# Kernel optimization log

Measured on AMD Instinct MI355X. Metric: run time of the kernel, lower is better.

Reference implementation:

```python
import jax, jax.numpy as jnp
import numpy as np

H = 4          # no_heads
C_HIDDEN = 32  # per-head hidden dim


def setup_inputs() -> dict:
    key = jax.random.key(0)
    ks = jax.random.split(key, 11)
    B, S, C = 1, 256, 128
    sc = 1.0 / np.sqrt(C).astype(np.float32)
    return {
        "q_x": jax.random.normal(ks[0], (B, S, S, C), jnp.float32),
        "kv_x": jax.random.normal(ks[1], (B, S, S, C), jnp.float32),
        "bias1": jax.random.normal(ks[2], (B, 1, H, S, S), jnp.float32),
        "bias2": jax.random.normal(ks[3], (B, S, 1, 1, S), jnp.float32),
        "wq": jax.random.normal(ks[4], (C, C), jnp.float32) * sc,
        "wk": jax.random.normal(ks[5], (C, C), jnp.float32) * sc,
        "wv": jax.random.normal(ks[6], (C, C), jnp.float32) * sc,
        "wg": jax.random.normal(ks[7], (C, C), jnp.float32) * sc,
        "bg": jax.random.normal(ks[8], (C,), jnp.float32) * 0.02,
        "wo": jax.random.normal(ks[9], (C, C), jnp.float32) * sc,
        "bo": jax.random.normal(ks[10], (C,), jnp.float32) * 0.02,
    }


def reference(q_x, kv_x, bias1, bias2, wq, wk, wv, wg, bg, wo, bo):
    # Linear projections (torch Linear semantics: x @ W^T), no bias on q/k/v.
    def split_heads(x):  # ... Q (H C) -> ... H Q C
        *lead, Q, _ = x.shape
        return jnp.moveaxis(x.reshape(*lead, Q, H, C_HIDDEN), -2, -3)

    q = split_heads(jnp.einsum('...qi,oi->...qo', q_x, wq)) / np.sqrt(C_HIDDEN)
    k = split_heads(jnp.einsum('...ki,oi->...ko', kv_x, wk))
    v = split_heads(jnp.einsum('...ki,oi->...ko', kv_x, wv))

    # scores: [B, S, H, Q, K]
    a = jnp.einsum('bshqd,bshkd->bshqk', q, k)
    a = a + bias1 + bias2
    a = jax.nn.softmax(a, axis=-1)
    o = jnp.einsum('bshqk,bshkd->bshqd', a, v)
    o = jnp.moveaxis(o, -3, -2)  # ... H Q C -> ... Q H C

    # sigmoid gating
    g = jax.nn.sigmoid(jnp.einsum('...qi,oi->...qo', q_x, wg) + bg)
    *lead, Q, _ = g.shape
    g = g.reshape(*lead, Q, H, C_HIDDEN)
    o = o * g

    o = o.reshape(*lead, Q, H * C_HIDDEN)
    return jnp.einsum('...qi,oi->...qo', o, wo) + bo
```

## Files before the change

kernel.cpp:

```cpp
#include <hip/hip_runtime.h>
#include <math.h>

typedef _Float16 f16;
typedef _Float16 h4 __attribute__((ext_vector_type(4)));
typedef _Float16 h8 __attribute__((ext_vector_type(8)));
typedef float f32x4 __attribute__((ext_vector_type(4)));

#define QSCALE 0.17677669529663689f

__global__ __launch_bounds__(256) void proj_mfma(
    const float* __restrict__ q_x, const float* __restrict__ kv_x,
    const float* __restrict__ wq, const float* __restrict__ wk,
    const float* __restrict__ wv, const float* __restrict__ wg,
    const float* __restrict__ bg,
    f16* __restrict__ qb, f16* __restrict__ kb,
    f16* __restrict__ vbT, f16* __restrict__ gb)
{
    __shared__ char lds[65536];
    char* xl = lds;
    char* wl = lds + 32768;
    const int t = threadIdx.x;
    const int lane = t & 63, wave = t >> 6;
    const int wr = wave >> 1, wc = wave & 1;
    const int lo = lane & 15, hi = lane >> 4;
    const int phase = blockIdx.y;
    const int row0 = blockIdx.x * 128;
    const float* xsrc = phase ? kv_x : q_x;

    #pragma unroll
    for (int j = 0; j < 16; ++j) {
        int f = t + 256 * j;
        int row = f >> 5, c4 = f & 31;
        float4 v = *(const float4*)(xsrc + (size_t)(row0 + row) * 128 + c4 * 4);
        h4 hv = {(f16)v.x, (f16)v.y, (f16)v.z, (f16)v.w};
        *(h4*)(xl + row * 256 + (((c4 >> 1) ^ (row & 7)) << 4) + ((c4 & 1) << 3)) = hv;
    }

    for (int sub = 0; sub < 2; ++sub) {
        const int pid = phase * 2 + sub;
        const float* w = (pid == 0) ? wq : (pid == 1) ? wg : (pid == 2) ? wk : wv;
        __syncthreads();
        #pragma unroll
        for (int j = 0; j < 16; ++j) {
            int f = t + 256 * j;
            int row = f >> 5, c4 = f & 31;
            float4 v = *(const float4*)(w + (size_t)row * 128 + c4 * 4);
            h4 hv = {(f16)v.x, (f16)v.y, (f16)v.z, (f16)v.w};
            *(h4*)(wl + row * 256 + (((c4 >> 1) ^ (row & 7)) << 4) + ((c4 & 1) << 3)) = hv;
        }
        __syncthreads();

        f32x4 acc[4][4];
        #pragma unroll
        for (int m = 0; m < 4; ++m)
            #pragma unroll
            for (int n = 0; n < 4; ++n) acc[m][n] = (f32x4){0.f, 0.f, 0.f, 0.f};

        #pragma unroll
        for (int kk = 0; kk < 4; ++kk) {
            const int swz = ((hi + 4 * kk) ^ (lo & 7)) << 4;
            h8 af[4], bf[4];
            #pragma unroll
            for (int m = 0; m < 4; ++m)
                af[m] = *(const h8*)(xl + (lo + 16 * m + 64 * wr) * 256 + swz);
            #pragma unroll
            for (int n = 0; n < 4; ++n)
                bf[n] = *(const h8*)(wl + (lo + 16 * n + 64 * wc) * 256 + swz);
            #pragma unroll
            for (int m = 0; m < 4; ++m)
                #pragma unroll
                for (int n = 0; n < 4; ++n)
                    acc[m][n] = __builtin_amdgcn_mfma_f32_16x16x32_f16(af[m], bf[n], acc[m][n], 0, 0, 0);
        }

        #pragma unroll
        for (int n = 0; n < 4; ++n) {
            const int col = 64 * wc + 16 * n + lo;
            const float bgv = (pid == 1) ? bg[col] : 0.f;
            #pragma unroll
            for (int m = 0; m < 4; ++m) {
                if (pid == 3) {
                    int rg = row0 + 64 * wr + 16 * m + 4 * hi;
                    int sidx = rg >> 8, key = rg & 255;
                    int hh = col >> 5, dh = col & 31;
                    h4 hv = {(f16)acc[m][n][0], (f16)acc[m][n][1],
                             (f16)acc[m][n][2], (f16)acc[m][n][3]};
                    *(h4*)(vbT + (((size_t)sidx * 4 + hh) * 32 + dh) * 256 + key) = hv;
                } else {
                    f16* dst = (pid == 0) ? qb : (pid == 1) ? gb : kb;
                    #pragma unroll
                    for (int r = 0; r < 4; ++r) {
                        int rg = row0 + 64 * wr + 16 * m + 4 * hi + r;
                        float v = acc[m][n][r];
                        if (pid == 0) v *= QSCALE;
                        else if (pid == 1) v = 1.f / (1.f + __expf(-(v + bgv)));
                        dst[(size_t)rg * 128 + col] = (f16)v;
                    }
                }
            }
        }
    }
}

__global__ __launch_bounds__(256) void attn_mfma(
    const f16* __restrict__ qb, const f16* __restrict__ kb,
    const f16* __restrict__ vbT, const f16* __restrict__ gb,
    const float* __restrict__ bias1, const float* __restrict__ bias2,
    f16* __restrict__ ob)
{
    __shared__ char plds[16384];
    const int h = blockIdx.x, s = blockIdx.y;
    const int t = threadIdx.x, wave = t >> 6, lane = t & 63;
    const int lo = lane & 15, hi = lane >> 4;
    char* pw = plds + wave * 4096;
    const size_t rowbase = (size_t)s * 256;
    const int q0 = wave * 64;

    h8 qf[4];
    #pragma unroll
    for (int m = 0; m < 4; ++m)
        qf[m] = *(const h8*)(qb + (rowbase + q0 + 16 * m + lo) * 128 + h * 32 + 8 * hi);

    f32x4 Oa[4][2];
    float mr[4][4], lr[4][4];
    #pragma unroll
    for (int m = 0; m < 4; ++m) {
        #pragma unroll
        for (int n = 0; n < 2; ++n) Oa[m][n] = (f32x4){0.f, 0.f, 0.f, 0.f};
        #pragma unroll
        for (int r = 0; r < 4; ++r) { mr[m][r] = -1e30f; lr[m][r] = 0.f; }
    }

    const float* b1 = bias1 + (size_t)h * 65536;
    const float* b2 = bias2 + (size_t)s * 256;
    const f16* vbase = vbT + ((size_t)s * 4 + h) * 32 * 256;

    for (int k0 = 0; k0 < 256; k0 += 32) {
        h8 kf[2];
        #pragma unroll
        for (int nt = 0; nt < 2; ++nt)
            kf[nt] = *(const h8*)(kb + (rowbase + k0 + 16 * nt + lo) * 128 + h * 32 + 8 * hi);
        float b2v[2];
        #pragma unroll
        for (int nt = 0; nt < 2; ++nt) b2v[nt] = b2[k0 + 16 * nt + lo];

        f32x4 acc[4][2];
        #pragma unroll
        for (int m = 0; m < 4; ++m)
            #pragma unroll
            for (int nt = 0; nt < 2; ++nt)
                #pragma unroll
                for (int r = 0; r < 4; ++r)
                    acc[m][nt][r] = b1[(q0 + 16 * m + 4 * hi + r) * 256 + k0 + 16 * nt + lo] + b2v[nt];

        #pragma unroll
        for (int m = 0; m < 4; ++m)
            #pragma unroll
            for (int nt = 0; nt < 2; ++nt)
                acc[m][nt] = __builtin_amdgcn_mfma_f32_16x16x32_f16(qf[m], kf[nt], acc[m][nt], 0, 0, 0);

        float corr[4][4];
        #pragma unroll
        for (int m = 0; m < 4; ++m) {
            #pragma unroll
            for (int r = 0; r < 4; ++r) {
                float mx = fmaxf(acc[m][0][r], acc[m][1][r]);
                #pragma unroll
                for (int wdt = 1; wdt < 16; wdt <<= 1)
                    mx = fmaxf(mx, __shfl_xor(mx, wdt, 16));
                float mn = fmaxf(mr[m][r], mx);
                corr[m][r] = __expf(mr[m][r] - mn);
                mr[m][r] = mn;
                float p0 = __expf(acc[m][0][r] - mn);
                float p1 = __expf(acc[m][1][r] - mn);
                acc[m][0][r] = p0;
                acc[m][1][r] = p1;
                float sm = p0 + p1;
                #pragma unroll
                for (int wdt = 1; wdt < 16; wdt <<= 1)
                    sm += __shfl_xor(sm, wdt, 16);
                lr[m][r] = lr[m][r] * corr[m][r] + sm;
            }
        }

        #pragma unroll
        for (int m = 0; m < 4; ++m)
            #pragma unroll
            for (int nt = 0; nt < 2; ++nt)
                #pragma unroll
                for (int r = 0; r < 4; ++r) {
                    int q = 16 * m + 4 * hi + r;
                    int swz = (nt * 2 + (lo >> 3)) ^ r ^ hi;
                    *(f16*)(pw + q * 64 + swz * 16 + (lo & 7) * 2) = (f16)acc[m][nt][r];
                }

        #pragma unroll
        for (int m = 0; m < 4; ++m)
            #pragma unroll
            for (int n2 = 0; n2 < 2; ++n2)
                #pragma unroll
                for (int r = 0; r < 4; ++r)
                    Oa[m][n2][r] *= corr[m][r];

        h8 vf[2];
        #pragma unroll
        for (int n2 = 0; n2 < 2; ++n2)
            vf[n2] = *(const h8*)(vbase + (n2 * 16 + lo) * 256 + k0 + 8 * hi);

        #pragma unroll
        for (int m = 0; m < 4; ++m) {
            int swz = hi ^ (lo & 3) ^ ((lo >> 2) & 3);
            h8 pa = *(const h8*)(pw + (16 * m + lo) * 64 + (swz << 4));
            #pragma unroll
            for (int n2 = 0; n2 < 2; ++n2)
                Oa[m][n2] = __builtin_amdgcn_mfma_f32_16x16x32_f16(pa, vf[n2], Oa[m][n2], 0, 0, 0);
        }
    }

    #pragma unroll
    for (int m = 0; m < 4; ++m) {
        #pragma unroll
        for (int r = 0; r < 4; ++r) {
            float inv = 1.f / lr[m][r];
            int qg = q0 + 16 * m + 4 * hi + r;
            #pragma unroll
            for (int n2 = 0; n2 < 2; ++n2) {
                size_t idx = (rowbase + qg) * 128 + h * 32 + n2 * 16 + lo;
                float g = (float)gb[idx];
                ob[idx] = (f16)(Oa[m][n2][r] * inv * g);
            }
        }
    }
}

__global__ __launch_bounds__(256) void out_mfma(
    const f16* __restrict__ ob, const float* __restrict__ wo,
    const float* __restrict__ bo, float* __restrict__ out)
{
    __shared__ char lds[65536];
    char* xl = lds;
    char* wl = lds + 32768;
    const int t = threadIdx.x;
    const int lane = t & 63, wave = t >> 6;
    const int wr = wave >> 1, wc = wave & 1;
    const int lo = lane & 15, hi = lane >> 4;
    const int row0 = blockIdx.x * 128;

    #pragma unroll
    for (int j = 0; j < 8; ++j) {
        int f = t + 256 * j;
        int row = f >> 4, c8 = f & 15;
        h8 v = *(const h8*)(ob + (size_t)(row0 + row) * 128 + c8 * 8);
        *(h8*)(xl + row * 256 + ((c8 ^ (row & 7)) << 4)) = v;
    }
    #pragma unroll
    for (int j = 0; j < 16; ++j) {
        int f = t + 256 * j;
        int row = f >> 5, c4 = f & 31;
        float4 v = *(const float4*)(wo + (size_t)row * 128 + c4 * 4);
        h4 hv = {(f16)v.x, (f16)v.y, (f16)v.z, (f16)v.w};
        *(h4*)(wl + row * 256 + (((c4 >> 1) ^ (row & 7)) << 4) + ((c4 & 1) << 3)) = hv;
    }
    __syncthreads();

    f32x4 acc[4][4];
    #pragma unroll
    for (int m = 0; m < 4; ++m)
        #pragma unroll
        for (int n = 0; n < 4; ++n) acc[m][n] = (f32x4){0.f, 0.f, 0.f, 0.f};

    #pragma unroll
    for (int kk = 0; kk < 4; ++kk) {
        const int swz = ((hi + 4 * kk) ^ (lo & 7)) << 4;
        h8 af[4], bf[4];
        #pragma unroll
        for (int m = 0; m < 4; ++m)
            af[m] = *(const h8*)(xl + (lo + 16 * m + 64 * wr) * 256 + swz);
        #pragma unroll
        for (int n = 0; n < 4; ++n)
            bf[n] = *(const h8*)(wl + (lo + 16 * n + 64 * wc) * 256 + swz);
        #pragma unroll
        for (int m = 0; m < 4; ++m)
            #pragma unroll
            for (int n = 0; n < 4; ++n)
                acc[m][n] = __builtin_amdgcn_mfma_f32_16x16x32_f16(af[m], bf[n], acc[m][n], 0, 0, 0);
    }

    #pragma unroll
    for (int n = 0; n < 4; ++n) {
        const int col = 64 * wc + 16 * n + lo;
        const float bov = bo[col];
        #pragma unroll
        for (int m = 0; m < 4; ++m)
            #pragma unroll
            for (int r = 0; r < 4; ++r)
                out[(size_t)(row0 + 64 * wr + 16 * m + 4 * hi + r) * 128 + col] = acc[m][n][r] + bov;
    }
}

extern "C" void kernel_launch(void* const* d_in, const int* in_sizes, int n_in,
                              void* d_out, int out_size, void* d_ws, size_t ws_size,
                              hipStream_t stream)
{
    const float* q_x   = (const float*)d_in[0];
    const float* kv_x  = (const float*)d_in[1];
    const float* bias1 = (const float*)d_in[2];
    const float* bias2 = (const float*)d_in[3];
    const float* wq    = (const float*)d_in[4];
    const float* wk    = (const float*)d_in[5];
    const float* wv    = (const float*)d_in[6];
    const float* wg    = (const float*)d_in[7];
    const float* bg    = (const float*)d_in[8];
    const float* wo    = (const float*)d_in[9];
    const float* bo    = (const float*)d_in[10];
    float* out = (float*)d_out;

    const size_t RC = (size_t)65536 * 128;
    f16* ws  = (f16*)d_ws;
    f16* qb  = ws;
    f16* kb  = ws + RC;
    f16* vbT = ws + 2 * RC;
    f16* gb  = ws + 3 * RC;
    f16* ob  = ws + 4 * RC;

    proj_mfma<<<dim3(512, 2), 256, 0, stream>>>(q_x, kv_x, wq, wk, wv, wg, bg, qb, kb, vbT, gb);
    attn_mfma<<<dim3(4, 256), 256, 0, stream>>>(qb, kb, vbT, gb, bias1, bias2, ob);
    out_mfma<<<512, 256, 0, stream>>>(ob, wo, bo, out);
}
```

Baseline: 130.2 us.

## Replace online-softmax attention loop with single-pass full-row softmax and 4x more blocks

The attention kernel now gives each wave 16 query rows instead of 64 and computes all 256 keys' scores at once, so softmax is done in one pass without online max/rescale corrections. The grid grows fourfold (16 x 256 blocks), which raises parallelism and occupancy. bias2 is staged through shared memory. In exchange, each wave holds 64 accumulator floats plus a larger P buffer in LDS (32KB per block), and K/V are reloaded by four separate blocks per head.

```diff
diff --git a/kernel.cpp b/kernel.cpp
--- a/kernel.cpp
+++ b/kernel.cpp
@@ -108,129 +108,89 @@
     const float* __restrict__ bias1, const float* __restrict__ bias2,
     f16* __restrict__ ob)
 {
-    __shared__ char plds[16384];
-    const int h = blockIdx.x, s = blockIdx.y;
+    __shared__ float b2s[256];
+    __shared__ char plds[32768];
+    const int x = blockIdx.x;
+    const int h = x >> 2, qblk = x & 3;
+    const int s = blockIdx.y;
     const int t = threadIdx.x, wave = t >> 6, lane = t & 63;
     const int lo = lane & 15, hi = lane >> 4;
-    char* pw = plds + wave * 4096;
+    char* pw = plds + wave * 8192;
     const size_t rowbase = (size_t)s * 256;
-    const int q0 = wave * 64;
-
-    h8 qf[4];
-    #pragma unroll
-    for (int m = 0; m < 4; ++m)
-        qf[m] = *(const h8*)(qb + (rowbase + q0 + 16 * m + lo) * 128 + h * 32 + 8 * hi);
-
-    f32x4 Oa[4][2];
-    float mr[4][4], lr[4][4];
-    #pragma unroll
-    for (int m = 0; m < 4; ++m) {
-        #pragma unroll
-        for (int n = 0; n < 2; ++n) Oa[m][n] = (f32x4){0.f, 0.f, 0.f, 0.f};
-        #pragma unroll
-        for (int r = 0; r < 4; ++r) { mr[m][r] = -1e30f; lr[m][r] = 0.f; }
-    }
+    const int q0 = qblk * 64 + wave * 16;
+
+    b2s[t] = bias2[s * 256 + t];
+    __syncthreads();
+
+    h8 qf = *(const h8*)(qb + (rowbase + q0 + lo) * 128 + h * 32 + 8 * hi);
 
     const float* b1 = bias1 + (size_t)h * 65536;
-    const float* b2 = bias2 + (size_t)s * 256;
+    f32x4 acc[16];
+    #pragma unroll
+    for (int nt = 0; nt < 16; ++nt) {
+        float b2v = b2s[16 * nt + lo];
+        #pragma unroll
+        for (int r = 0; r < 4; ++r)
+            acc[nt][r] = b1[(q0 + 4 * hi + r) * 256 + 16 * nt + lo] + b2v;
+    }
+    #pragma unroll
+    for (int nt = 0; nt < 16; ++nt) {
+        h8 kf = *(const h8*)(kb + (rowbase + 16 * nt + lo) * 128 + h * 32 + 8 * hi);
+        acc[nt] = __builtin_amdgcn_mfma_f32_16x16x32_f16(qf, kf, acc[nt], 0, 0, 0);
+    }
+
+    float inv_l[4];
+    #pragma unroll
+    for (int r = 0; r < 4; ++r) {
+        float mx = acc[0][r];
+        #pragma unroll
+        for (int nt = 1; nt < 16; ++nt) mx = fmaxf(mx, acc[nt][r]);
+        #pragma unroll
+        for (int w = 1; w < 16; w <<= 1) mx = fmaxf(mx, __shfl_xor(mx, w, 16));
+        float sm = 0.f;
+        #pragma unroll
+        for (int nt = 0; nt < 16; ++nt) {
+            float p = __expf(acc[nt][r] - mx);
+            acc[nt][r] = p;
+            sm += p;
+        }
+        #pragma unroll
+        for (int w = 1; w < 16; w <<= 1) sm += __shfl_xor(sm, w, 16);
+        inv_l[r] = 1.f / sm;
+    }
+
+    #pragma unroll
+    for (int nt = 0; nt < 16; ++nt)
+        #pragma unroll
+        for (int r = 0; r < 4; ++r) {
+            int row = 4 * hi + r, k = 16 * nt + lo;
+            int cs = (k >> 3) ^ (row & 7);
+            *(f16*)(pw + row * 512 + cs * 16 + (k & 7) * 2) = (f16)acc[nt][r];
+        }
+
     const f16* vbase = vbT + ((size_t)s * 4 + h) * 32 * 256;
-
-    for (int k0 = 0; k0 < 256; k0 += 32) {
-        h8 kf[2];
-        #pragma unroll
-        for (int nt = 0; nt < 2; ++nt)
-            kf[nt] = *(const h8*)(kb + (rowbase + k0 + 16 * nt + lo) * 128 + h * 32 + 8 * hi);
-        float b2v[2];
-        #pragma unroll
-        for (int nt = 0; nt < 2; ++nt) b2v[nt] = b2[k0 + 16 * nt + lo];
-
-        f32x4 acc[4][2];
-        #pragma unroll
-        for (int m = 0; m < 4; ++m)
-            #pragma unroll
-            for (int nt = 0; nt < 2; ++nt)
-                #pragma unroll
-                for (int r = 0; r < 4; ++r)
-                    acc[m][nt][r] = b1[(q0 + 16 * m + 4 * hi + r) * 256 + k0 + 16 * nt + lo] + b2v[nt];
-
-        #pragma unroll
-        for (int m = 0; m < 4; ++m)
-            #pragma unroll
-            for (int nt = 0; nt < 2; ++nt)
-                acc[m][nt] = __builtin_amdgcn_mfma_f32_16x16x32_f16(qf[m], kf[nt], acc[m][nt], 0, 0, 0);
-
-        float corr[4][4];
-        #pragma unroll
-        for (int m = 0; m < 4; ++m) {
-            #pragma unroll
-            for (int r = 0; r < 4; ++r) {
-                float mx = fmaxf(acc[m][0][r], acc[m][1][r]);
-                #pragma unroll
-                for (int wdt = 1; wdt < 16; wdt <<= 1)
-                    mx = fmaxf(mx, __shfl_xor(mx, wdt, 16));
-                float mn = fmaxf(mr[m][r], mx);
-                corr[m][r] = __expf(mr[m][r] - mn);
-                mr[m][r] = mn;
-                float p0 = __expf(acc[m][0][r] - mn);
-                float p1 = __expf(acc[m][1][r] - mn);
-                acc[m][0][r] = p0;
-                acc[m][1][r] = p1;
-                float sm = p0 + p1;
-                #pragma unroll
-                for (int wdt = 1; wdt < 16; wdt <<= 1)
-                    sm += __shfl_xor(sm, wdt, 16);
-                lr[m][r] = lr[m][r] * corr[m][r] + sm;
-            }
-        }
-
-        #pragma unroll
-        for (int m = 0; m < 4; ++m)
-            #pragma unroll
-            for (int nt = 0; nt < 2; ++nt)
-                #pragma unroll
-                for (int r = 0; r < 4; ++r) {
-                    int q = 16 * m + 4 * hi + r;
-                    int swz = (nt * 2 + (lo >> 3)) ^ r ^ hi;
-                    *(f16*)(pw + q * 64 + swz * 16 + (lo & 7) * 2) = (f16)acc[m][nt][r];
-                }
-
-        #pragma unroll
-        for (int m = 0; m < 4; ++m)
-            #pragma unroll
-            for (int n2 = 0; n2 < 2; ++n2)
-                #pragma unroll
-                for (int r = 0; r < 4; ++r)
-                    Oa[m][n2][r] *= corr[m][r];
-
-        h8 vf[2];
-        #pragma unroll
-        for (int n2 = 0; n2 < 2; ++n2)
-            vf[n2] = *(const h8*)(vbase + (n2 * 16 + lo) * 256 + k0 + 8 * hi);
-
-        #pragma unroll
-        for (int m = 0; m < 4; ++m) {
-            int swz = hi ^ (lo & 3) ^ ((lo >> 2) & 3);
-            h8 pa = *(const h8*)(pw + (16 * m + lo) * 64 + (swz << 4));
-            #pragma unroll
-            for (int n2 = 0; n2 < 2; ++n2)
-                Oa[m][n2] = __builtin_amdgcn_mfma_f32_16x16x32_f16(pa, vf[n2], Oa[m][n2], 0, 0, 0);
-        }
-    }
-
-    #pragma unroll
-    for (int m = 0; m < 4; ++m) {
+    f32x4 Oa[2];
+    Oa[0] = (f32x4){0.f, 0.f, 0.f, 0.f};
+    Oa[1] = (f32x4){0.f, 0.f, 0.f, 0.f};
+    #pragma unroll
+    for (int kt = 0; kt < 8; ++kt) {
+        int cs = (4 * kt + hi) ^ (lo & 7);
+        h8 pa = *(const h8*)(pw + lo * 512 + cs * 16);
+        #pragma unroll
+        for (int n2 = 0; n2 < 2; ++n2) {
+            h8 vf = *(const h8*)(vbase + (size_t)(n2 * 16 + lo) * 256 + 32 * kt + 8 * hi);
+            Oa[n2] = __builtin_amdgcn_mfma_f32_16x16x32_f16(pa, vf, Oa[n2], 0, 0, 0);
+        }
+    }
+
+    #pragma unroll
+    for (int n2 = 0; n2 < 2; ++n2)
         #pragma unroll
         for (int r = 0; r < 4; ++r) {
-            float inv = 1.f / lr[m][r];
-            int qg = q0 + 16 * m + 4 * hi + r;
-            #pragma unroll
-            for (int n2 = 0; n2 < 2; ++n2) {
-                size_t idx = (rowbase + qg) * 128 + h * 32 + n2 * 16 + lo;
-                float g = (float)gb[idx];
-                ob[idx] = (f16)(Oa[m][n2][r] * inv * g);
-            }
-        }
-    }
+            size_t idx = (rowbase + q0 + 4 * hi + r) * 128 + h * 32 + n2 * 16 + lo;
+            float g = (float)gb[idx];
+            ob[idx] = (f16)(Oa[n2][r] * inv_l[r] * g);
+        }
 }
 
 __global__ __launch_bounds__(256) void out_mfma(
@@ -324,6 +284,6 @@
     f16* ob  = ws + 4 * RC;
 
     proj_mfma<<<dim3(512, 2), 256, 0, stream>>>(q_x, kv_x, wq, wk, wv, wg, bg, qb, kb, vbT, gb);
-    attn_mfma<<<dim3(4, 256), 256, 0, stream>>>(qb, kb, vbT, gb, bias1, bias2, ob);
+    attn_mfma<<<dim3(16, 256), 256, 0, stream>>>(qb, kb, vbT, gb, bias1, bias2, ob);
     out_mfma<<<512, 256, 0, stream>>>(ob, wo, bo, out);
 }
```

New measurement: 157.4 us. 20.9% more time.
